# Kernel tuning notes

Hardware: AMD Instinct MI355X
Metric: run time of the kernel (lower is better)

## Reference

```python
import jax, jax.numpy as jnp
import numpy as np

NUM_PERTS = 20000
D = 256          # embedding_dim
B, C = 64, 512   # batch_size, num_cells
EPS = 1e-5


def setup_inputs() -> dict:
    key = jax.random.key(0)
    ks = jax.random.split(key, 20)
    inp = {
        'perturbation_ids': jax.random.randint(ks[0], (B, C), 0, NUM_PERTS),
        'table': jax.random.normal(ks[1], (NUM_PERTS, D), dtype=jnp.float32),
    }
    s = 1.0 / np.sqrt(D)
    for i in range(4):
        inp[f'W{i+1}'] = jax.random.uniform(ks[2 + 2 * i], (D, D), minval=-s, maxval=s, dtype=jnp.float32)
        inp[f'b{i+1}'] = jax.random.uniform(ks[3 + 2 * i], (D,), minval=-s, maxval=s, dtype=jnp.float32)
    for i in range(3):
        inp[f'g{i+1}'] = jnp.ones((D,), jnp.float32)
        inp[f'be{i+1}'] = jnp.zeros((D,), jnp.float32)
    return inp


def _bn(x, gamma, beta):
    # BatchNorm1d forward with batch statistics (training-mode math, biased var)
    mu = jnp.mean(x, axis=0)
    var = jnp.mean(jnp.square(x - mu), axis=0)
    return (x - mu) * jax.lax.rsqrt(var + EPS) * gamma + beta


def reference(perturbation_ids, table,
              W1, b1, W2, b2, W3, b3, W4, b4,
              g1, be1, g2, be2, g3, be3):
    # Vectorized replacement of the Python double-loop dict gather
    emb = table[perturbation_ids]                 # (B, C, D)
    x = emb.reshape(-1, D)                        # (B*C, D)
    x = _bn(jax.nn.gelu(x @ W1 + b1, approximate=False), g1, be1)
    x = _bn(jax.nn.gelu(x @ W2 + b2, approximate=False), g2, be2)
    x = _bn(jax.nn.gelu(x @ W3 + b3, approximate=False), g3, be3)
    x = jax.nn.gelu(x @ W4 + b4, approximate=False)
    return x.reshape(B, C, D)
```

## Files before the change

kernel.cpp:

```cpp
#include <hip/hip_runtime.h>
#include <math.h>


typedef __attribute__((ext_vector_type(8))) short short8;
typedef __attribute__((ext_vector_type(4))) float floatx4;

#define DDIM 256

__device__ __forceinline__ unsigned short f2bf(float f) {
    union { float f; unsigned int u; } v; v.f = f;
    unsigned int r = v.u + 0x7fffu + ((v.u >> 16) & 1u);
    return (unsigned short)(r >> 16);
}
__device__ __forceinline__ float bf2f(unsigned short u) {
    union { unsigned int i; float f; } v; v.i = ((unsigned int)u) << 16;
    return v.f;
}
__device__ __forceinline__ float gelu_fast(float x) {
    float z = 0.7978845608f * (x + 0.044715f * x * x * x);
    float e = __expf(2.0f * z);
    float th = 1.0f - 2.0f * __builtin_amdgcn_rcpf(1.0f + e);
    return 0.5f * x * (1.0f + th);
}

__global__ void prep_kernel(const float* __restrict__ W0,
                            const float* __restrict__ W1,
                            const float* __restrict__ W2,
                            const float* __restrict__ W3,
                            unsigned short* __restrict__ Wt ,
                            float* __restrict__ stats )
{
    const int t = threadIdx.x, b = blockIdx.x;
    const int j = b >> 8, n = b & 255;
    const float* W = (j == 0) ? W0 : (j == 1) ? W1 : (j == 2) ? W2 : W3;
    Wt[((size_t)j << 16) + (size_t)t * DDIM + n] = f2bf(W[(size_t)n * DDIM + t]);
    if (b < 12) {
        float* s = stats + b * 1024;
        s[t] = 0.f; s[t + 256] = 0.f; s[t + 512] = 0.f; s[t + 768] = 0.f;
    }
}

template<int GATHER, int AFFINE, int WRITE_F32, int DO_STATS>
__global__ __launch_bounds__(256, 2)
void gemm_enc(const unsigned short* __restrict__ A,
              const int* __restrict__ ids,
              const float* __restrict__ table,
              const unsigned short* __restrict__ Wt,
              const float* __restrict__ bias,
              const float* __restrict__ statsIn,
              const float* __restrict__ gma,
              const float* __restrict__ bta,
              void* __restrict__ outp,
              float* __restrict__ statShards)
{
    __shared__ alignas(16) unsigned short Albs[64 * 256];
    __shared__ float sc[256], sh[256];

    const int tid  = threadIdx.x;
    const int blk  = blockIdx.x;
    const int wave = tid >> 6;
    const int lane = tid & 63;
    const int quad = lane >> 4;
    const int l15  = lane & 15;
    const int wn   = wave;
    const int row0 = blk * 64;

    if (AFFINE) {
        float sum = 0.f, sq = 0.f;
#pragma unroll
        for (int s = 0; s < 8; ++s) {
            sum += statsIn[s * 512 + tid];
            sq  += statsIn[s * 512 + 256 + tid];
        }
        const float mu  = sum * (1.f / 32768.f);
        const float var = sq * (1.f / 32768.f) - mu * mu;
        const float scl = rsqrtf(var + 1e-5f) * gma[tid];
        sc[tid] = scl;
        sh[tid] = bta[tid] - mu * scl;
        __syncthreads();
    }

    {
        const int r  = tid >> 2;
        const int c0 = (tid & 3) * 64;
        if (GATHER) {
            const int src = ids[row0 + r];
            const float* tp = table + (size_t)src * DDIM + c0;
#pragma unroll
            for (int j = 0; j < 8; ++j) {
                float4 v0 = *(const float4*)(tp + j * 8);
                float4 v1 = *(const float4*)(tp + j * 8 + 4);
                union { unsigned short u[8]; uint4 v; } o;
                o.u[0]=f2bf(v0.x); o.u[1]=f2bf(v0.y); o.u[2]=f2bf(v0.z); o.u[3]=f2bf(v0.w);
                o.u[4]=f2bf(v1.x); o.u[5]=f2bf(v1.y); o.u[6]=f2bf(v1.z); o.u[7]=f2bf(v1.w);
                const int g = (tid & 3) * 8 + j;
                *(uint4*)(Albs + r * 256 + (g ^ (r & 7)) * 8) = o.v;
            }
        } else {
            const unsigned short* ap = A + (size_t)(row0 + r) * DDIM + c0;
#pragma unroll
            for (int j = 0; j < 8; ++j) {
                union { unsigned short u[8]; uint4 v; } o;
                o.v = *(const uint4*)(ap + j * 8);
                if (AFFINE) {
#pragma unroll
                    for (int e = 0; e < 8; ++e) {
                        const int c = c0 + j * 8 + e;
                        o.u[e] = f2bf(fmaf(bf2f(o.u[e]), sc[c], sh[c]));
                    }
                }
                const int g = (tid & 3) * 8 + j;
                *(uint4*)(Albs + r * 256 + (g ^ (r & 7)) * 8) = o.v;
            }
        }
    }

    float bias_v[4];
#pragma unroll
    for (int nt = 0; nt < 4; ++nt)
        bias_v[nt] = bias[wn * 64 + nt * 16 + l15];

    floatx4 acc[4][4];
#pragma unroll
    for (int i = 0; i < 4; ++i)
#pragma unroll
        for (int j = 0; j < 4; ++j)
            acc[i][j] = floatx4{0.f, 0.f, 0.f, 0.f};

    __syncthreads();

    const unsigned short* wb = Wt + (size_t)(wn * 64 + l15) * DDIM + quad * 8;
    short8 bfr[4], bnx[4], af[4], anx[4];
    {
        const int agp = (quad ^ (l15 & 7)) * 8;
#pragma unroll
        for (int nt = 0; nt < 4; ++nt)
            bfr[nt] = *(const short8*)(wb + (size_t)(nt * 16) * DDIM);
#pragma unroll
        for (int mt = 0; mt < 4; ++mt)
            af[mt] = *(const short8*)(Albs + (mt * 16 + l15) * 256 + agp);
    }
#pragma unroll
    for (int kk = 0; kk < 8; ++kk) {
        if (kk < 7) {
            const int agp = (((kk + 1) * 4 + quad) ^ (l15 & 7)) * 8;
#pragma unroll
            for (int nt = 0; nt < 4; ++nt)
                bnx[nt] = *(const short8*)(wb + (size_t)(nt * 16) * DDIM
                                           + (kk + 1) * 32);
#pragma unroll
            for (int mt = 0; mt < 4; ++mt)
                anx[mt] = *(const short8*)(Albs + (mt * 16 + l15) * 256 + agp);
        }
#pragma unroll
        for (int mt = 0; mt < 4; ++mt)
#pragma unroll
            for (int nt = 0; nt < 4; ++nt)
                acc[mt][nt] = __builtin_amdgcn_mfma_f32_16x16x32_bf16(
                    af[mt], bfr[nt], acc[mt][nt], 0, 0, 0);
#pragma unroll
        for (int x = 0; x < 4; ++x) { af[x] = anx[x]; bfr[x] = bnx[x]; }
    }

    float s1[4] = {0.f, 0.f, 0.f, 0.f};
    float s2[4] = {0.f, 0.f, 0.f, 0.f};
#pragma unroll
    for (int mt = 0; mt < 4; ++mt) {
        const int rb = row0 + mt * 16 + quad * 4;
#pragma unroll
        for (int nt = 0; nt < 4; ++nt) {
            const int col = wn * 64 + nt * 16 + l15;
#pragma unroll
            for (int i = 0; i < 4; ++i) {
                float y = gelu_fast(acc[mt][nt][i] + bias_v[nt]);
                if (WRITE_F32) {
                    ((float*)outp)[(size_t)(rb + i) * DDIM + col] = y;
                } else {
                    ((unsigned short*)outp)[(size_t)(rb + i) * DDIM + col] = f2bf(y);
                }
                if (DO_STATS) { s1[nt] += y; s2[nt] += y * y; }
            }
        }
    }
    if (DO_STATS) {
#pragma unroll
        for (int nt = 0; nt < 4; ++nt) {
            s1[nt] += __shfl_xor(s1[nt], 16); s1[nt] += __shfl_xor(s1[nt], 32);
            s2[nt] += __shfl_xor(s2[nt], 16); s2[nt] += __shfl_xor(s2[nt], 32);
        }
        float* sb = statShards + (blk & 7) * 512;
        if (quad == 0) {
#pragma unroll
            for (int nt = 0; nt < 4; ++nt) {
                const int col = wn * 64 + nt * 16 + l15;
                atomicAdd(&sb[col],       s1[nt]);
                atomicAdd(&sb[256 + col], s2[nt]);
            }
        }
    }
}

extern "C" void kernel_launch(void* const* d_in, const int* in_sizes, int n_in,
                              void* d_out, int out_size, void* d_ws, size_t ws_size,
                              hipStream_t stream)
{
    const int*   ids   = (const int*)  d_in[0];
    const float* table = (const float*)d_in[1];
    const float* W1 = (const float*)d_in[2];  const float* b1 = (const float*)d_in[3];
    const float* W2 = (const float*)d_in[4];  const float* b2 = (const float*)d_in[5];
    const float* W3 = (const float*)d_in[6];  const float* b3 = (const float*)d_in[7];
    const float* W4 = (const float*)d_in[8];  const float* b4 = (const float*)d_in[9];
    const float* g1 = (const float*)d_in[10]; const float* be1 = (const float*)d_in[11];
    const float* g2 = (const float*)d_in[12]; const float* be2 = (const float*)d_in[13];
    const float* g3 = (const float*)d_in[14]; const float* be3 = (const float*)d_in[15];

    unsigned char* ws = (unsigned char*)d_ws;
    unsigned short* Wt   = (unsigned short*)ws;
    float* stats = (float*)(ws + (size_t)524288);
    unsigned short* act1 = (unsigned short*)(ws + (size_t)1048576);
    unsigned short* act2 = (unsigned short*)(ws + (size_t)17825792);
    unsigned short* Wt1 = Wt;
    unsigned short* Wt2 = Wt + 65536;
    unsigned short* Wt3 = Wt + 131072;
    unsigned short* Wt4 = Wt + 196608;

    prep_kernel<<<1024, 256, 0, stream>>>(W1, W2, W3, W4, Wt, stats);

    gemm_enc<1, 0, 0, 1><<<512, 256, 0, stream>>>(
        nullptr, ids, table, Wt1, b1, nullptr, nullptr, nullptr, act1, stats);
    gemm_enc<0, 1, 0, 1><<<512, 256, 0, stream>>>(
        act1, nullptr, nullptr, Wt2, b2, stats, g1, be1, act2, stats + 4096);
    gemm_enc<0, 1, 0, 1><<<512, 256, 0, stream>>>(
        act2, nullptr, nullptr, Wt3, b3, stats + 4096, g2, be2, act1, stats + 8192);
    gemm_enc<0, 1, 1, 0><<<512, 256, 0, stream>>>(
        act1, nullptr, nullptr, Wt4, b4, stats + 8192, g3, be3, (void*)d_out, nullptr);
}
```

Baseline: 183.9 us.

## Fuse all layers into one persistent kernel with grid barriers and LDS-resident activations

Merges the weight-prep kernel and the four GEMM layers into one launch of 512 blocks. Grid-wide atomic barriers stand in for the kernel boundaries, and each block keeps its 64-row activation tile in shared memory across layers, so the intermediate bf16 activations no longer round-trip through global memory. This removes launch gaps and activation traffic. In exchange it relies on all 512 blocks being co-resident (two per CU via launch bounds), adds spin-wait barrier cost, and uses a capped spin that could break out early and silently break correctness.

Result: slower. 524.0 us (+184.9%).

```diff
diff --git a/kernel.cpp b/kernel.cpp
--- a/kernel.cpp
+++ b/kernel.cpp
@@ -6,6 +6,20 @@
 typedef __attribute__((ext_vector_type(4))) float floatx4;
 
 #define DDIM 256
+#define NBLK 512
+
+struct Params {
+    const int* ids;
+    const float* table;
+    const float* W[4];
+    const float* b[4];
+    const float* g[3];
+    const float* be[3];
+    unsigned short* Wt;
+    float* stats;
+    unsigned int* barrier;
+    float* out;
+};
 
 __device__ __forceinline__ unsigned short f2bf(float f) {
     union { float f; unsigned int u; } v; v.f = f;
@@ -23,39 +37,32 @@
     return 0.5f * x * (1.0f + th);
 }
 
-__global__ void prep_kernel(const float* __restrict__ W0,
-                            const float* __restrict__ W1,
-                            const float* __restrict__ W2,
-                            const float* __restrict__ W3,
-                            unsigned short* __restrict__ Wt ,
-                            float* __restrict__ stats )
-{
-    const int t = threadIdx.x, b = blockIdx.x;
-    const int j = b >> 8, n = b & 255;
-    const float* W = (j == 0) ? W0 : (j == 1) ? W1 : (j == 2) ? W2 : W3;
-    Wt[((size_t)j << 16) + (size_t)t * DDIM + n] = f2bf(W[(size_t)n * DDIM + t]);
-    if (b < 12) {
-        float* s = stats + b * 1024;
-        s[t] = 0.f; s[t + 256] = 0.f; s[t + 512] = 0.f; s[t + 768] = 0.f;
-    }
-}
-
-template<int GATHER, int AFFINE, int WRITE_F32, int DO_STATS>
-__global__ __launch_bounds__(256, 2)
-void gemm_enc(const unsigned short* __restrict__ A,
-              const int* __restrict__ ids,
-              const float* __restrict__ table,
-              const unsigned short* __restrict__ Wt,
-              const float* __restrict__ bias,
-              const float* __restrict__ statsIn,
-              const float* __restrict__ gma,
-              const float* __restrict__ bta,
-              void* __restrict__ outp,
-              float* __restrict__ statShards)
-{
-    __shared__ alignas(16) unsigned short Albs[64 * 256];
-    __shared__ float sc[256], sh[256];
-
+__device__ __forceinline__ void grid_barrier(unsigned int* cnt)
+{
+    __threadfence();
+    __syncthreads();
+    if (threadIdx.x == 0) {
+        __hip_atomic_fetch_add(cnt, 1u, __ATOMIC_ACQ_REL,
+                               __HIP_MEMORY_SCOPE_AGENT);
+        int cap = 2000000;
+        while (__hip_atomic_load(cnt, __ATOMIC_ACQUIRE,
+                                 __HIP_MEMORY_SCOPE_AGENT) < (unsigned)NBLK) {
+            __builtin_amdgcn_s_sleep(2);
+            if (--cap == 0) break;
+        }
+    }
+    __syncthreads();
+    __threadfence();
+}
+
+template<int GATHER, int AFFINE, int LAST>
+__device__ __forceinline__ void layer_step(
+    unsigned short* P, float* sc, float* sh,
+    const Params& p,
+    const unsigned short* Wt, const float* bias,
+    const float* statsIn, const float* gma, const float* bta,
+    float* statShards)
+{
     const int tid  = threadIdx.x;
     const int blk  = blockIdx.x;
     const int wave = tid >> 6;
@@ -69,8 +76,10 @@
         float sum = 0.f, sq = 0.f;
 #pragma unroll
         for (int s = 0; s < 8; ++s) {
-            sum += statsIn[s * 512 + tid];
-            sq  += statsIn[s * 512 + 256 + tid];
+            sum += __hip_atomic_load(&statsIn[s * 512 + tid],
+                                     __ATOMIC_RELAXED, __HIP_MEMORY_SCOPE_AGENT);
+            sq  += __hip_atomic_load(&statsIn[s * 512 + 256 + tid],
+                                     __ATOMIC_RELAXED, __HIP_MEMORY_SCOPE_AGENT);
         }
         const float mu  = sum * (1.f / 32768.f);
         const float var = sq * (1.f / 32768.f) - mu * mu;
@@ -84,8 +93,8 @@
         const int r  = tid >> 2;
         const int c0 = (tid & 3) * 64;
         if (GATHER) {
-            const int src = ids[row0 + r];
-            const float* tp = table + (size_t)src * DDIM + c0;
+            const int src = p.ids[row0 + r];
+            const float* tp = p.table + (size_t)src * DDIM + c0;
 #pragma unroll
             for (int j = 0; j < 8; ++j) {
                 float4 v0 = *(const float4*)(tp + j * 8);
@@ -94,23 +103,21 @@
                 o.u[0]=f2bf(v0.x); o.u[1]=f2bf(v0.y); o.u[2]=f2bf(v0.z); o.u[3]=f2bf(v0.w);
                 o.u[4]=f2bf(v1.x); o.u[5]=f2bf(v1.y); o.u[6]=f2bf(v1.z); o.u[7]=f2bf(v1.w);
                 const int g = (tid & 3) * 8 + j;
-                *(uint4*)(Albs + r * 256 + (g ^ (r & 7)) * 8) = o.v;
+                *(uint4*)(P + r * 256 + ((g ^ (r & 7)) << 3)) = o.v;
             }
         } else {
-            const unsigned short* ap = A + (size_t)(row0 + r) * DDIM + c0;
 #pragma unroll
             for (int j = 0; j < 8; ++j) {
+                const int g = (tid & 3) * 8 + j;
+                unsigned short* slot = P + r * 256 + ((g ^ (r & 7)) << 3);
                 union { unsigned short u[8]; uint4 v; } o;
-                o.v = *(const uint4*)(ap + j * 8);
-                if (AFFINE) {
-#pragma unroll
-                    for (int e = 0; e < 8; ++e) {
-                        const int c = c0 + j * 8 + e;
-                        o.u[e] = f2bf(fmaf(bf2f(o.u[e]), sc[c], sh[c]));
-                    }
+                o.v = *(const uint4*)slot;
+#pragma unroll
+                for (int e = 0; e < 8; ++e) {
+                    const int c = c0 + j * 8 + e;
+                    o.u[e] = f2bf(fmaf(bf2f(o.u[e]), sc[c], sh[c]));
                 }
-                const int g = (tid & 3) * 8 + j;
-                *(uint4*)(Albs + r * 256 + (g ^ (r & 7)) * 8) = o.v;
+                *(uint4*)slot = o.v;
             }
         }
     }
@@ -138,7 +145,7 @@
             bfr[nt] = *(const short8*)(wb + (size_t)(nt * 16) * DDIM);
 #pragma unroll
         for (int mt = 0; mt < 4; ++mt)
-            af[mt] = *(const short8*)(Albs + (mt * 16 + l15) * 256 + agp);
+            af[mt] = *(const short8*)(P + (mt * 16 + l15) * 256 + agp);
     }
 #pragma unroll
     for (int kk = 0; kk < 8; ++kk) {
@@ -150,7 +157,7 @@
                                            + (kk + 1) * 32);
 #pragma unroll
             for (int mt = 0; mt < 4; ++mt)
-                anx[mt] = *(const short8*)(Albs + (mt * 16 + l15) * 256 + agp);
+                anx[mt] = *(const short8*)(P + (mt * 16 + l15) * 256 + agp);
         }
 #pragma unroll
         for (int mt = 0; mt < 4; ++mt)
@@ -162,27 +169,30 @@
         for (int x = 0; x < 4; ++x) { af[x] = anx[x]; bfr[x] = bnx[x]; }
     }
 
+    if (!LAST) __syncthreads();
+
     float s1[4] = {0.f, 0.f, 0.f, 0.f};
     float s2[4] = {0.f, 0.f, 0.f, 0.f};
 #pragma unroll
     for (int mt = 0; mt < 4; ++mt) {
-        const int rb = row0 + mt * 16 + quad * 4;
 #pragma unroll
         for (int nt = 0; nt < 4; ++nt) {
             const int col = wn * 64 + nt * 16 + l15;
 #pragma unroll
             for (int i = 0; i < 4; ++i) {
+                const int r = mt * 16 + quad * 4 + i;
                 float y = gelu_fast(acc[mt][nt][i] + bias_v[nt]);
-                if (WRITE_F32) {
-                    ((float*)outp)[(size_t)(rb + i) * DDIM + col] = y;
+                if (LAST) {
+                    p.out[(size_t)(row0 + r) * DDIM + col] = y;
                 } else {
-                    ((unsigned short*)outp)[(size_t)(rb + i) * DDIM + col] = f2bf(y);
+                    const int g = col >> 3;
+                    P[r * 256 + ((g ^ (r & 7)) << 3) + (col & 7)] = f2bf(y);
+                    s1[nt] += y; s2[nt] += y * y;
                 }
-                if (DO_STATS) { s1[nt] += y; s2[nt] += y * y; }
-            }
-        }
-    }
-    if (DO_STATS) {
+            }
+        }
+    }
+    if (!LAST) {
 #pragma unroll
         for (int nt = 0; nt < 4; ++nt) {
             s1[nt] += __shfl_xor(s1[nt], 16); s1[nt] += __shfl_xor(s1[nt], 32);
@@ -200,38 +210,62 @@
     }
 }
 
+__global__ __launch_bounds__(256, 2) void fused_enc(Params p)
+{
+    __shared__ alignas(16) unsigned short P[64 * 256];
+    __shared__ float sc[256], sh[256];
+
+    const int tid = threadIdx.x, blk = blockIdx.x;
+
+    {
+        const int j  = blk >> 7;
+        const int n0 = (blk & 127) * 2;
+        const float* W = p.W[j];
+        unsigned short* dst = p.Wt + ((size_t)j << 16);
+        dst[(size_t)tid * DDIM + n0]     = f2bf(W[(size_t)n0 * DDIM + tid]);
+        dst[(size_t)tid * DDIM + n0 + 1] = f2bf(W[(size_t)(n0 + 1) * DDIM + tid]);
+        if (blk < 12) {
+            float* s = p.stats + blk * 1024;
+            s[tid] = 0.f; s[tid + 256] = 0.f; s[tid + 512] = 0.f; s[tid + 768] = 0.f;
+        }
+    }
+    grid_barrier(p.barrier + 0);
+
+    layer_step<1, 0, 0>(P, sc, sh, p, p.Wt,          p.b[0],
+                        nullptr,         nullptr, nullptr, p.stats);
+    grid_barrier(p.barrier + 1);
+    layer_step<0, 1, 0>(P, sc, sh, p, p.Wt + 65536,  p.b[1],
+                        p.stats,         p.g[0],  p.be[0], p.stats + 4096);
+    grid_barrier(p.barrier + 2);
+    layer_step<0, 1, 0>(P, sc, sh, p, p.Wt + 131072, p.b[2],
+                        p.stats + 4096,  p.g[1],  p.be[1], p.stats + 8192);
+    grid_barrier(p.barrier + 3);
+    layer_step<0, 1, 1>(P, sc, sh, p, p.Wt + 196608, p.b[3],
+                        p.stats + 8192,  p.g[2],  p.be[2], nullptr);
+}
+
 extern "C" void kernel_launch(void* const* d_in, const int* in_sizes, int n_in,
                               void* d_out, int out_size, void* d_ws, size_t ws_size,
                               hipStream_t stream)
 {
-    const int*   ids   = (const int*)  d_in[0];
-    const float* table = (const float*)d_in[1];
-    const float* W1 = (const float*)d_in[2];  const float* b1 = (const float*)d_in[3];
-    const float* W2 = (const float*)d_in[4];  const float* b2 = (const float*)d_in[5];
-    const float* W3 = (const float*)d_in[6];  const float* b3 = (const float*)d_in[7];
-    const float* W4 = (const float*)d_in[8];  const float* b4 = (const float*)d_in[9];
-    const float* g1 = (const float*)d_in[10]; const float* be1 = (const float*)d_in[11];
-    const float* g2 = (const float*)d_in[12]; const float* be2 = (const float*)d_in[13];
-    const float* g3 = (const float*)d_in[14]; const float* be3 = (const float*)d_in[15];
+    Params pp;
+    pp.ids   = (const int*)  d_in[0];
+    pp.table = (const float*)d_in[1];
+    pp.W[0] = (const float*)d_in[2];  pp.b[0] = (const float*)d_in[3];
+    pp.W[1] = (const float*)d_in[4];  pp.b[1] = (const float*)d_in[5];
+    pp.W[2] = (const float*)d_in[6];  pp.b[2] = (const float*)d_in[7];
+    pp.W[3] = (const float*)d_in[8];  pp.b[3] = (const float*)d_in[9];
+    pp.g[0] = (const float*)d_in[10]; pp.be[0] = (const float*)d_in[11];
+    pp.g[1] = (const float*)d_in[12]; pp.be[1] = (const float*)d_in[13];
+    pp.g[2] = (const float*)d_in[14]; pp.be[2] = (const float*)d_in[15];
 
     unsigned char* ws = (unsigned char*)d_ws;
-    unsigned short* Wt   = (unsigned short*)ws;
-    float* stats = (float*)(ws + (size_t)524288);
-    unsigned short* act1 = (unsigned short*)(ws + (size_t)1048576);
-    unsigned short* act2 = (unsigned short*)(ws + (size_t)17825792);
-    unsigned short* Wt1 = Wt;
-    unsigned short* Wt2 = Wt + 65536;
-    unsigned short* Wt3 = Wt + 131072;
-    unsigned short* Wt4 = Wt + 196608;
-
-    prep_kernel<<<1024, 256, 0, stream>>>(W1, W2, W3, W4, Wt, stats);
-
-    gemm_enc<1, 0, 0, 1><<<512, 256, 0, stream>>>(
-        nullptr, ids, table, Wt1, b1, nullptr, nullptr, nullptr, act1, stats);
-    gemm_enc<0, 1, 0, 1><<<512, 256, 0, stream>>>(
-        act1, nullptr, nullptr, Wt2, b2, stats, g1, be1, act2, stats + 4096);
-    gemm_enc<0, 1, 0, 1><<<512, 256, 0, stream>>>(
-        act2, nullptr, nullptr, Wt3, b3, stats + 4096, g2, be2, act1, stats + 8192);
-    gemm_enc<0, 1, 1, 0><<<512, 256, 0, stream>>>(
-        act1, nullptr, nullptr, Wt4, b4, stats + 8192, g3, be3, (void*)d_out, nullptr);
-}
+    pp.Wt      = (unsigned short*)ws;
+    pp.stats   = (float*)(ws + (size_t)524288);
+    pp.barrier = (unsigned int*)(ws + (size_t)589824);
+    pp.out     = (float*)d_out;
+
+    hipMemsetAsync(ws + (size_t)589824, 0, 16, stream);
+
+    fused_enc<<<dim3(NBLK), dim3(256), 0, stream>>>(pp);
+}
```
